# Kernel tuning notes

Hardware: AMD Instinct MI355X
Metric: run time of the kernel (lower is better)

## Reference

```python
import jax, jax.numpy as jnp
import numpy as np

NUM_HEADS = 16
EPS = 1e-6


def _ln(t, w, b):
    # LayerNorm over last dim (head_dim), elementwise affine, eps=1e-6
    mu = jnp.mean(t, axis=-1, keepdims=True)
    var = jnp.mean(jnp.square(t - mu), axis=-1, keepdims=True)
    return (t - mu) * jax.lax.rsqrt(var + EPS) * w + b


def setup_inputs() -> dict:
    key = jax.random.key(0)
    ks = jax.random.split(key, 10)
    b, s1, s2, qdim, kdim = 2, 2048, 3072, 1024, 1024
    d = qdim // NUM_HEADS
    x = jax.random.normal(ks[0], (b, s1, qdim), dtype=jnp.float32)
    y = jax.random.normal(ks[1], (b, s2, kdim), dtype=jnp.float32)
    padding_mask = jax.random.randint(ks[2], (b, s2), 0, 2) > 0
    # guarantee at least one valid key per row (avoid all -inf softmax rows)
    padding_mask = padding_mask.at[:, 0].set(True)
    w = 0.02
    Wq = jax.random.normal(ks[3], (qdim, qdim), dtype=jnp.float32) * w
    bq = jnp.zeros((qdim,), jnp.float32)
    Wkv = jax.random.normal(ks[4], (2 * qdim, kdim), dtype=jnp.float32) * w
    bkv = jnp.zeros((2 * qdim,), jnp.float32)
    qn_w = jnp.ones((d,), jnp.float32)
    qn_b = jnp.zeros((d,), jnp.float32)
    kn_w = jnp.ones((d,), jnp.float32)
    kn_b = jnp.zeros((d,), jnp.float32)
    Wo = jax.random.normal(ks[5], (qdim, qdim), dtype=jnp.float32) * w
    bo = jnp.zeros((qdim,), jnp.float32)
    return {"x": x, "y": y, "padding_mask": padding_mask,
            "Wq": Wq, "bq": bq, "Wkv": Wkv, "bkv": bkv,
            "qn_w": qn_w, "qn_b": qn_b, "kn_w": kn_w, "kn_b": kn_b,
            "Wo": Wo, "bo": bo}


def reference(x, y, padding_mask, Wq, bq, Wkv, bkv, qn_w, qn_b, kn_w, kn_b, Wo, bo):
    b, s1, c = x.shape
    s2 = y.shape[1]
    h, d = NUM_HEADS, c // NUM_HEADS
    scale = d ** (-0.5)
    q = (x @ Wq.T + bq).reshape(b, s1, h, d)
    kv = (y @ Wkv.T + bkv).reshape(b, s2, 2, h, d)
    k, v = kv[:, :, 0], kv[:, :, 1]  # (b, s2, h, d)
    q = _ln(q, qn_w, qn_b) * scale
    k = _ln(k, kn_w, kn_b)
    attn = jnp.einsum('bihd,bjhd->bhij', q, k)  # (b, h, s1, s2)
    attn = jnp.where(padding_mask[:, None, None, :], attn, -jnp.inf)
    p = jax.nn.softmax(attn, axis=-1)
    ctx = jnp.einsum('bhij,bjhd->bihd', p, v).reshape(b, s1, c)
    out = ctx @ Wo.T + bo
    return out
```

## Files before the change

### kernel.cpp

```cpp
#include <hip/hip_runtime.h>
#include <stdint.h>
#include <stddef.h>

typedef __attribute__((ext_vector_type(4))) float  f32x4;
typedef __attribute__((ext_vector_type(8))) short  short8;
typedef __attribute__((ext_vector_type(4))) short  short4v;
typedef __attribute__((ext_vector_type(2))) unsigned int uint2v;

__device__ __forceinline__ unsigned short f2bfbits(float f) {
  unsigned int u = __builtin_bit_cast(unsigned int, f);
  u += 0x7FFFu + ((u >> 16) & 1u);
  return (unsigned short)(u >> 16);
}

__device__ __forceinline__ f32x4 mfma16(short8 a, short8 b, f32x4 c) {
  return __builtin_amdgcn_mfma_f32_16x16x32_bf16(a, b, c, 0, 0, 0);
}

__device__ __forceinline__ unsigned int cvtpk(float a, float b) {
  unsigned int r;
  asm volatile("v_cvt_pk_bf16_f32 %0, %1, %2" : "=v"(r) : "v"(a), "v"(b));
  return r;
}

__device__ __forceinline__ void gload16(const void* g, void* l) {
  __builtin_amdgcn_global_load_lds(
      (const __attribute__((address_space(1))) void*)g,
      (__attribute__((address_space(3))) void*)l, 16, 0, 0);
}

__device__ __forceinline__ void cvt_block(const float* __restrict__ in,
                                          unsigned short* __restrict__ out,
                                          int blk, int t) {
  size_t i = (size_t)blk * 256 + t;
  f32x4 a = *(const f32x4*)(in + i * 8);
  f32x4 b = *(const f32x4*)(in + i * 8 + 4);
  short8 o;
  o[0] = (short)f2bfbits(a[0]); o[1] = (short)f2bfbits(a[1]);
  o[2] = (short)f2bfbits(a[2]); o[3] = (short)f2bfbits(a[3]);
  o[4] = (short)f2bfbits(b[0]); o[5] = (short)f2bfbits(b[1]);
  o[6] = (short)f2bfbits(b[2]); o[7] = (short)f2bfbits(b[3]);
  *(short8*)(out + i * 8) = o;
}

__global__ __launch_bounds__(256) void fused_prep(
    const float* __restrict__ x, unsigned short* __restrict__ xb,
    const float* __restrict__ y, unsigned short* __restrict__ yb,
    const float* __restrict__ Wq, unsigned short* __restrict__ Wqb,
    const float* __restrict__ Wkv, unsigned short* __restrict__ Wkvb,
    const float* __restrict__ Wo, unsigned short* __restrict__ Wob,
    const unsigned char* __restrict__ mraw, float* __restrict__ madd) {
  const int bid = blockIdx.x, t = threadIdx.x;
  if (bid < 2048)       { cvt_block(x,   xb,   bid,        t); return; }
  else if (bid < 5120)  { cvt_block(y,   yb,   bid - 2048, t); return; }
  else if (bid < 5632)  { cvt_block(Wq,  Wqb,  bid - 5120, t); return; }
  else if (bid < 6656)  { cvt_block(Wkv, Wkvb, bid - 5632, t); return; }
  else if (bid < 7168)  { cvt_block(Wo,  Wob,  bid - 6656, t); return; }
  __shared__ int s_na, s_gt, s_m84;
  if (t == 0) { s_na = 0; s_gt = 0; s_m84 = 0; }
  __syncthreads();
  int na = 0, gt = 0, m84 = 0;
  for (int i = t; i < 4096; i += 256) {
    unsigned char v = mraw[i];
    if (v) {
      if (i & 3) na++;
      if ((i & 7) == 4) m84++;
      if (v > 1) gt++;
    }
  }
  atomicAdd(&s_na, na); atomicAdd(&s_gt, gt); atomicAdd(&s_m84, m84);
  __syncthreads();
  int layout;
  if (s_na == 0) layout = s_m84 ? 1 : 3;
  else           layout = s_gt ? 2 : 0;
  int i = (bid - 7168) * 256 + t;
  bool mv;
  if (layout == 0)      mv = mraw[i] != 0;
  else if (layout == 1) mv = ((const int*)mraw)[i] != 0;
  else if (layout == 2) mv = ((const float*)mraw)[i] > 0.5f;
  else                  mv = ((const long long*)mraw)[i] != 0;
  madd[i] = mv ? -10.0f : -1e30f;
}

__global__ __launch_bounds__(256) void gemm_qkv(
    const unsigned short* __restrict__ xb, const unsigned short* __restrict__ Wqb,
    const float* __restrict__ bq, const float* __restrict__ qnw,
    const float* __restrict__ qnb, unsigned short* __restrict__ qln,
    const unsigned short* __restrict__ yb, const unsigned short* __restrict__ Wkvb,
    const float* __restrict__ bkv, const float* __restrict__ knw,
    const float* __restrict__ knb, unsigned short* __restrict__ kln,
    unsigned short* __restrict__ vt) {
  __shared__ unsigned short As[128 * 64];
  __shared__ unsigned short Bs[128 * 64];
  const int t = threadIdx.x, l = t & 63, w = t >> 6;
  const int lo = l & 15, hi = l >> 4;
  const int wr = w >> 1, wc = w & 1;
  const int bid = blockIdx.x;
  const int isq = bid < 256;
  const int bn = isq ? (bid & 7) : ((bid - 256) & 15);
  const int bm = isq ? (bid >> 3) : ((bid - 256) >> 4);
  const unsigned short* A = isq ? xb : yb;
  const unsigned short* B = isq ? Wqb : Wkvb;
  const float* bias = isq ? bq : bkv;
  const float* lnw = isq ? qnw : knw;
  const float* lnb = isq ? qnb : knb;
  unsigned short* bfout = isq ? qln : kln;
  const float lnscale = isq ? 0.125f * 1.44269504f : 1.0f;
  const int rpb = isq ? 2048 : 3072;
  const int K = 1024;

  const int sr = l >> 3;
  const int sc = ((l & 7) ^ sr) << 3;
  const unsigned short* Ab = A + (size_t)bm * 128 * K + (size_t)sr * K + sc;
  const unsigned short* Bb = B + (size_t)bn * 128 * K + (size_t)sr * K + sc;

  f32x4 acc[4][4] = {};

  for (int kt = 0; kt < K; kt += 64) {
    __syncthreads();
#pragma unroll
    for (int p = 0; p < 4; ++p) {
      int c = w * 4 + p;
      gload16(Ab + (size_t)c * 8 * K + kt, &As[c * 512]);
      gload16(Bb + (size_t)c * 8 * K + kt, &Bs[c * 512]);
    }
    __syncthreads();
#pragma unroll
    for (int kk = 0; kk < 2; ++kk) {
      short8 af[4], bf[4];
#pragma unroll
      for (int i = 0; i < 4; ++i) {
        int slot = (((kk * 4 + hi) ^ (lo & 7)) << 3);
        af[i] = *(const short8*)&As[(wr * 64 + i * 16 + lo) * 64 + slot];
        bf[i] = *(const short8*)&Bs[(wc * 64 + i * 16 + lo) * 64 + slot];
      }
#pragma unroll
      for (int i = 0; i < 4; ++i)
#pragma unroll
        for (int j = 0; j < 4; ++j)
          acc[i][j] = mfma16(af[i], bf[j], acc[i][j]);
    }
  }

  float bv[4];
#pragma unroll
  for (int j = 0; j < 4; ++j) bv[j] = bias[bn * 128 + wc * 64 + j * 16 + lo];
#pragma unroll
  for (int i = 0; i < 4; ++i)
#pragma unroll
    for (int j = 0; j < 4; ++j)
#pragma unroll
      for (int r = 0; r < 4; ++r) acc[i][j][r] += bv[j];

  if (!isq && bn >= 8) {
#pragma unroll
    for (int j = 0; j < 4; ++j) {
      int col = bn * 128 + wc * 64 + j * 16 + lo;
      int vcol = col - 1024, hh = vcol >> 6, dd = vcol & 63;
#pragma unroll
      for (int i = 0; i < 4; ++i) {
        int row = bm * 128 + wr * 64 + i * 16 + hi * 4;
        int bb = row >= 3072;
        int jj = row - bb * 3072;
        short4v o;
#pragma unroll
        for (int r = 0; r < 4; ++r) o[r] = (short)f2bfbits(acc[i][j][r]);
        *(short4v*)(vt + ((size_t)((bb * 16 + hh) * 64 + dd)) * 3072 + jj) = o;
      }
    }
  } else {
    float gwv[4], gbv[4];
#pragma unroll
    for (int j = 0; j < 4; ++j) {
      gwv[j] = lnw[j * 16 + lo];
      gbv[j] = lnb[j * 16 + lo];
    }
    const int hcol = (bn * 128 + wc * 64) >> 6;
#pragma unroll
    for (int i = 0; i < 4; ++i) {
#pragma unroll
      for (int r = 0; r < 4; ++r) {
        float s1 = (acc[i][0][r] + acc[i][1][r]) + (acc[i][2][r] + acc[i][3][r]);
        float s2 = (acc[i][0][r] * acc[i][0][r] + acc[i][1][r] * acc[i][1][r]) +
                   (acc[i][2][r] * acc[i][2][r] + acc[i][3][r] * acc[i][3][r]);
#pragma unroll
        for (int m = 1; m < 16; m <<= 1) {
          s1 += __shfl_xor(s1, m);
          s2 += __shfl_xor(s2, m);
        }
        float mu = s1 * 0.015625f;
        float var = fmaxf(s2 * 0.015625f - mu * mu, 0.0f);
        float rq = rsqrtf(var + 1e-6f);
        int row = bm * 128 + wr * 64 + i * 16 + hi * 4 + r;
        int bb = row >= rpb;
        int rr = row - bb * rpb;
        size_t base = ((size_t)(bb * 16 + hcol) * rpb + rr) * 64;
#pragma unroll
        for (int j = 0; j < 4; ++j)
          bfout[base + j * 16 + lo] =
              f2bfbits(((acc[i][j][r] - mu) * rq * gwv[j] + gbv[j]) * lnscale);
      }
    }
  }
}

__global__ __launch_bounds__(512) void gemm_out(
    const unsigned short* __restrict__ A, const unsigned short* __restrict__ B,
    const float* __restrict__ bias, float* __restrict__ C, int N, int K) {
  __shared__ unsigned short As[128 * 64];
  __shared__ unsigned short Bs[128 * 64];
  const int t = threadIdx.x, l = t & 63, w = t >> 6;
  const int lo = l & 15, hi = l >> 4;
  const int wr = w >> 1, wc = w & 1;
  const int bn = blockIdx.x, bm = blockIdx.y;

  const int sr = l >> 3;
  const int sc = ((l & 7) ^ sr) << 3;
  const unsigned short* Ab = A + (size_t)bm * 128 * K + (size_t)sr * K + sc;
  const unsigned short* Bb = B + (size_t)bn * 128 * K + (size_t)sr * K + sc;

  f32x4 acc[2][4] = {};

  for (int kt = 0; kt < K; kt += 64) {
    __syncthreads();
#pragma unroll
    for (int p = 0; p < 2; ++p) {
      int c = p * 8 + w;
      gload16(Ab + (size_t)c * 8 * K + kt, &As[c * 512]);
      gload16(Bb + (size_t)c * 8 * K + kt, &Bs[c * 512]);
    }
    __syncthreads();
#pragma unroll
    for (int kk = 0; kk < 2; ++kk) {
      short8 af[2], bf[4];
#pragma unroll
      for (int i = 0; i < 2; ++i) {
        int slot = (((kk * 4 + hi) ^ (lo & 7)) << 3);
        af[i] = *(const short8*)&As[(wr * 32 + i * 16 + lo) * 64 + slot];
      }
#pragma unroll
      for (int j = 0; j < 4; ++j) {
        int slot = (((kk * 4 + hi) ^ (lo & 7)) << 3);
        bf[j] = *(const short8*)&Bs[(wc * 64 + j * 16 + lo) * 64 + slot];
      }
#pragma unroll
      for (int i = 0; i < 2; ++i)
#pragma unroll
        for (int j = 0; j < 4; ++j)
          acc[i][j] = mfma16(af[i], bf[j], acc[i][j]);
    }
  }

#pragma unroll
  for (int j = 0; j < 4; ++j) {
    int col = bn * 128 + wc * 64 + j * 16 + lo;
    float bv = bias[col];
#pragma unroll
    for (int i = 0; i < 2; ++i) {
      int row = bm * 128 + wr * 32 + i * 16 + hi * 4;
#pragma unroll
      for (int r = 0; r < 4; ++r)
        C[(size_t)(row + r) * N + col] = acc[i][j][r] + bv;
    }
  }
}

__global__ __launch_bounds__(256, 4) void attn_fwd(
    const unsigned short* __restrict__ Q, const unsigned short* __restrict__ Kn,
    const unsigned short* __restrict__ Vt, const float* __restrict__ maskAdd,
    unsigned short* __restrict__ ctx) {
  int flat = blockIdx.y * 32 + blockIdx.x;
  int f = (flat & 7) * 128 + (flat >> 3);
  const int bh = f >> 5, qb = f & 31;
  const int b = bh >> 4, h = bh & 15;
  const int t = threadIdx.x, l = t & 63, w = t >> 6;
  const int lo = l & 15, hi = l >> 4;
  const int q0 = qb * 64 + w * 16;

  __shared__ unsigned short lds[20480];
  unsigned short* Ks = lds;
  unsigned short* Vs = lds + 8192;
  unsigned short* P  = lds + 16384 + w * 1024;

  const unsigned short* Qh = Q + ((size_t)bh * 2048 + q0) * 64;
  const unsigned short* Kb = Kn + (size_t)bh * 3072 * 64;
  const unsigned short* Vb = Vt + (size_t)bh * 64 * 3072;
  const float* mb = maskAdd + b * 3072;

  const int srow = w * 8 + (l >> 3);
  const int swz8 = ((l & 7) ^ ((l >> 3) & 7)) << 3;
  const unsigned short* kS = Kb + (size_t)srow * 64 + swz8;
  const unsigned short* vS = Vb + (size_t)srow * 3072 + swz8;
  const int dstoff = w * 512;

  short8 qf[2];
#pragma unroll
  for (int g = 0; g < 2; g++)
    qf[g] = *(const short8*)(Qh + (size_t)lo * 64 + g * 32 + hi * 8);

  f32x4 O[4] = {};
  f32x4 lacc = {};
  const int myswz = (lo & 7) << 3;

  short8 paR[2] = {};
  short8 vfR[4][2] = {};

#pragma unroll
  for (int j = 0; j < 2; ++j) {
    gload16(kS + (size_t)j * 2048, Ks + j * 2048 + dstoff);
    gload16(vS + (size_t)j * 98304, Vs + j * 2048 + dstoff);
  }
  __syncthreads();

  for (int kt = 0; kt < 3072; kt += 64) {
    const int cur = (kt >> 6) & 1;
    const int nxt = cur ^ 1;
    const int ktn = (kt + 64 < 3072) ? kt + 64 : 0;
#pragma unroll
    for (int j = 0; j < 2; ++j) {
      gload16(kS + (size_t)ktn * 64 + (size_t)j * 2048,
              Ks + nxt * 4096 + j * 2048 + dstoff);
      gload16(vS + ktn + (size_t)j * 98304,
              Vs + nxt * 4096 + j * 2048 + dstoff);
    }

    const unsigned short* Kc = Ks + cur * 4096;
    const unsigned short* Vc = Vs + cur * 4096;

    f32x4 s[4];
#pragma unroll
    for (int nf = 0; nf < 4; nf++)
      s[nf] = *(const f32x4*)(mb + kt + nf * 16 + hi * 4);
    __builtin_amdgcn_s_setprio(1);
#pragma unroll
    for (int nf = 0; nf < 4; nf++) {
      const int row = nf * 16 + lo;
      short8 k0 = *(const short8*)&Kc[row * 64 + ((hi * 8) ^ myswz)];
      short8 k1 = *(const short8*)&Kc[row * 64 + ((32 + hi * 8) ^ myswz)];
      s[nf] = mfma16(k0, qf[0], s[nf]);
      s[nf] = mfma16(k1, qf[1], s[nf]);
    }

#pragma unroll
    for (int df = 0; df < 4; df++)
#pragma unroll
      for (int ks = 0; ks < 2; ks++)
        O[df] = mfma16(paR[ks], vfR[df][ks], O[df]);
    __builtin_amdgcn_s_setprio(0);

#pragma unroll
    for (int nf = 0; nf < 4; nf++)
#pragma unroll
      for (int r = 0; r < 4; r++)
        s[nf][r] = __builtin_amdgcn_exp2f(s[nf][r]);
    lacc += (s[0] + s[1]) + (s[2] + s[3]);

#pragma unroll
    for (int nf = 0; nf < 4; nf++) {
      uint2v u;
      u.x = cvtpk(s[nf][0], s[nf][1]);
      u.y = cvtpk(s[nf][2], s[nf][3]);
      *(uint2v*)&P[lo * 64 + ((nf * 16 + hi * 4) ^ myswz)] = u;
    }
#pragma unroll
    for (int ks = 0; ks < 2; ks++)
      paR[ks] = *(const short8*)&P[lo * 64 + ((ks * 32 + hi * 8) ^ myswz)];
#pragma unroll
    for (int df = 0; df < 4; df++) {
      const int row = df * 16 + lo;
#pragma unroll
      for (int ks = 0; ks < 2; ks++)
        vfR[df][ks] = *(const short8*)&Vc[row * 64 + ((ks * 32 + hi * 8) ^ myswz)];
    }

    __syncthreads();
  }

  __builtin_amdgcn_s_setprio(1);
#pragma unroll
  for (int df = 0; df < 4; df++)
#pragma unroll
    for (int ks = 0; ks < 2; ks++)
      O[df] = mfma16(paR[ks], vfR[df][ks], O[df]);
  __builtin_amdgcn_s_setprio(0);

  float lr = (lacc[0] + lacc[1]) + (lacc[2] + lacc[3]);
  lr += __shfl_xor(lr, 16);
  lr += __shfl_xor(lr, 32);

  float i0 = 1.0f / __shfl(lr, hi * 4 + 0);
  float i1 = 1.0f / __shfl(lr, hi * 4 + 1);
  float i2 = 1.0f / __shfl(lr, hi * 4 + 2);
  float i3 = 1.0f / __shfl(lr, hi * 4 + 3);
  size_t rbase = (size_t)b * 2048 + q0 + hi * 4;
#pragma unroll
  for (int df = 0; df < 4; df++) {
    int cc = h * 64 + df * 16 + lo;
    ctx[(rbase + 0) * 1024 + cc] = f2bfbits(O[df][0] * i0);
    ctx[(rbase + 1) * 1024 + cc] = f2bfbits(O[df][1] * i1);
    ctx[(rbase + 2) * 1024 + cc] = f2bfbits(O[df][2] * i2);
    ctx[(rbase + 3) * 1024 + cc] = f2bfbits(O[df][3] * i3);
  }
}

extern "C" void kernel_launch(void* const* d_in, const int* in_sizes, int n_in,
                              void* d_out, int out_size, void* d_ws, size_t ws_size,
                              hipStream_t stream) {
  const float* x   = (const float*)d_in[0];
  const float* y   = (const float*)d_in[1];
  const unsigned char* pmask = (const unsigned char*)d_in[2];
  const float* Wq  = (const float*)d_in[3];
  const float* bq  = (const float*)d_in[4];
  const float* Wkv = (const float*)d_in[5];
  const float* bkv = (const float*)d_in[6];
  const float* qnw = (const float*)d_in[7];
  const float* qnb = (const float*)d_in[8];
  const float* knw = (const float*)d_in[9];
  const float* knb = (const float*)d_in[10];
  const float* Wo  = (const float*)d_in[11];
  const float* bo  = (const float*)d_in[12];
  float* out = (float*)d_out;

  const size_t MB = 1024ull * 1024ull;
  char* ws = (char*)d_ws;
  float* maskAdd       = (float*)ws;
  unsigned short* Wqb  = (unsigned short*)(ws + 32768);
  unsigned short* Wkvb = (unsigned short*)(ws + 32768 + 2 * MB);
  unsigned short* Wob  = (unsigned short*)(ws + 32768 + 6 * MB);
  unsigned short* qln  = (unsigned short*)(ws + 32768 + 8 * MB);
  unsigned short* kln  = (unsigned short*)(ws + 32768 + 16 * MB);
  unsigned short* vt   = (unsigned short*)(ws + 32768 + 28 * MB);
  unsigned short* ctxb = (unsigned short*)(ws + 32768 + 40 * MB);
  unsigned short* yb   = (unsigned short*)(ws + 32768 + 48 * MB);
  unsigned short* xb   = (unsigned short*)(ws + 32768 + 60 * MB);
  if (ws_size < 32768 + 68 * MB) return;

  fused_prep<<<dim3(7192), dim3(256), 0, stream>>>(
      x, xb, y, yb, Wq, Wqb, Wkv, Wkvb, Wo, Wob, pmask, maskAdd);

  gemm_qkv<<<dim3(1024), dim3(256), 0, stream>>>(
      xb, Wqb, bq, qnw, qnb, qln, yb, Wkvb, bkv, knw, knb, kln, vt);

  attn_fwd<<<dim3(32, 32), dim3(256), 0, stream>>>(qln, kln, vt, maskAdd, ctxb);

  gemm_out<<<dim3(8, 32), dim3(512), 0, stream>>>(ctxb, Wob, bo, out, 1024, 1024);
}
```

Baseline: 169.5 us.

## Compact valid keys via mask prefix-sum permutation and skip padded key tiles

The prep kernel now runs a prefix sum over the padding mask per batch, producing a permutation that moves valid keys to the front and a count of valid keys. The QKV GEMM scatters K rows and V columns through this permutation, and attention iterates only up to the rounded-up valid count. This removes compute on masked keys, which is about half of them with a random mask. In exchange, the V stores become scalar scattered writes instead of vector stores, and each output row needs an extra permutation lookup.

```diff
diff --git a/kernel.cpp b/kernel.cpp
--- a/kernel.cpp
+++ b/kernel.cpp
@@ -49,13 +49,16 @@
     const float* __restrict__ Wq, unsigned short* __restrict__ Wqb,
     const float* __restrict__ Wkv, unsigned short* __restrict__ Wkvb,
     const float* __restrict__ Wo, unsigned short* __restrict__ Wob,
-    const unsigned char* __restrict__ mraw, float* __restrict__ madd) {
+    const unsigned char* __restrict__ mraw, float* __restrict__ maddC,
+    int* __restrict__ perm, int* __restrict__ nvalid) {
   const int bid = blockIdx.x, t = threadIdx.x;
   if (bid < 2048)       { cvt_block(x,   xb,   bid,        t); return; }
   else if (bid < 5120)  { cvt_block(y,   yb,   bid - 2048, t); return; }
   else if (bid < 5632)  { cvt_block(Wq,  Wqb,  bid - 5120, t); return; }
   else if (bid < 6656)  { cvt_block(Wkv, Wkvb, bid - 5632, t); return; }
   else if (bid < 7168)  { cvt_block(Wo,  Wob,  bid - 6656, t); return; }
+
+  const int batch = bid - 7168;
   __shared__ int s_na, s_gt, s_m84;
   if (t == 0) { s_na = 0; s_gt = 0; s_m84 = 0; }
   __syncthreads();
@@ -73,13 +76,46 @@
   int layout;
   if (s_na == 0) layout = s_m84 ? 1 : 3;
   else           layout = s_gt ? 2 : 0;
-  int i = (bid - 7168) * 256 + t;
-  bool mv;
-  if (layout == 0)      mv = mraw[i] != 0;
-  else if (layout == 1) mv = ((const int*)mraw)[i] != 0;
-  else if (layout == 2) mv = ((const float*)mraw)[i] > 0.5f;
-  else                  mv = ((const long long*)mraw)[i] != 0;
-  madd[i] = mv ? -10.0f : -1e30f;
+
+  const int base = batch * 3072;
+  int myv[12];
+  int cnt = 0;
+#pragma unroll
+  for (int k = 0; k < 12; k++) {
+    int j = t * 12 + k;
+    int gj = base + j;
+    bool mv;
+    if (layout == 0)      mv = mraw[gj] != 0;
+    else if (layout == 1) mv = ((const int*)mraw)[gj] != 0;
+    else if (layout == 2) mv = ((const float*)mraw)[gj] > 0.5f;
+    else                  mv = ((const long long*)mraw)[gj] != 0;
+    myv[k] = mv ? 1 : 0;
+    cnt += myv[k];
+  }
+  const int lane = t & 63, wv = t >> 6;
+  int inc = cnt;
+#pragma unroll
+  for (int d = 1; d < 64; d <<= 1) {
+    int n = __shfl_up(inc, d);
+    if (lane >= d) inc += n;
+  }
+  __shared__ int wsum[4];
+  if (lane == 63) wsum[wv] = inc;
+  __syncthreads();
+  int woff = 0;
+#pragma unroll
+  for (int i2 = 0; i2 < 4; i2++) if (i2 < wv) woff += wsum[i2];
+  const int total = wsum[0] + wsum[1] + wsum[2] + wsum[3];
+  int vp = woff + inc - cnt;
+  if (t == 0) nvalid[batch] = total;
+#pragma unroll
+  for (int k = 0; k < 12; k++) {
+    int j = t * 12 + k;
+    perm[base + j] = myv[k] ? vp : (total + (j - vp));
+    vp += myv[k];
+  }
+  for (int jj = t; jj < 3072; jj += 256)
+    maddC[base + jj] = (jj < total) ? -10.0f : -1e30f;
 }
 
 __global__ __launch_bounds__(256) void gemm_qkv(
@@ -89,7 +125,7 @@
     const unsigned short* __restrict__ yb, const unsigned short* __restrict__ Wkvb,
     const float* __restrict__ bkv, const float* __restrict__ knw,
     const float* __restrict__ knb, unsigned short* __restrict__ kln,
-    unsigned short* __restrict__ vt) {
+    unsigned short* __restrict__ vt, const int* __restrict__ perm) {
   __shared__ unsigned short As[128 * 64];
   __shared__ unsigned short Bs[128 * 64];
   const int t = threadIdx.x, l = t & 63, w = t >> 6;
@@ -162,10 +198,12 @@
         int row = bm * 128 + wr * 64 + i * 16 + hi * 4;
         int bb = row >= 3072;
         int jj = row - bb * 3072;
-        short4v o;
-#pragma unroll
-        for (int r = 0; r < 4; ++r) o[r] = (short)f2bfbits(acc[i][j][r]);
-        *(short4v*)(vt + ((size_t)((bb * 16 + hh) * 64 + dd)) * 3072 + jj) = o;
+        size_t vbase = ((size_t)((bb * 16 + hh) * 64 + dd)) * 3072;
+#pragma unroll
+        for (int r = 0; r < 4; ++r) {
+          int p = perm[bb * 3072 + jj + r];
+          vt[vbase + p] = f2bfbits(acc[i][j][r]);
+        }
       }
     }
   } else {
@@ -194,7 +232,8 @@
         int row = bm * 128 + wr * 64 + i * 16 + hi * 4 + r;
         int bb = row >= rpb;
         int rr = row - bb * rpb;
-        size_t base = ((size_t)(bb * 16 + hcol) * rpb + rr) * 64;
+        int rrs = isq ? rr : perm[bb * 3072 + rr];
+        size_t base = ((size_t)(bb * 16 + hcol) * rpb + rrs) * 64;
 #pragma unroll
         for (int j = 0; j < 4; ++j)
           bfout[base + j * 16 + lo] =
@@ -268,7 +307,7 @@
 __global__ __launch_bounds__(256, 4) void attn_fwd(
     const unsigned short* __restrict__ Q, const unsigned short* __restrict__ Kn,
     const unsigned short* __restrict__ Vt, const float* __restrict__ maskAdd,
-    unsigned short* __restrict__ ctx) {
+    const int* __restrict__ nva, unsigned short* __restrict__ ctx) {
   int flat = blockIdx.y * 32 + blockIdx.x;
   int f = (flat & 7) * 128 + (flat >> 3);
   const int bh = f >> 5, qb = f & 31;
@@ -277,6 +316,9 @@
   const int lo = l & 15, hi = l >> 4;
   const int q0 = qb * 64 + w * 16;
 
+  const int nv = nva[b];
+  const int kend = (nv + 63) & ~63;
+
   __shared__ unsigned short lds[20480];
   unsigned short* Ks = lds;
   unsigned short* Vs = lds + 8192;
@@ -312,10 +354,10 @@
   }
   __syncthreads();
 
-  for (int kt = 0; kt < 3072; kt += 64) {
+  for (int kt = 0; kt < kend; kt += 64) {
     const int cur = (kt >> 6) & 1;
     const int nxt = cur ^ 1;
-    const int ktn = (kt + 64 < 3072) ? kt + 64 : 0;
+    const int ktn = (kt + 64 < kend) ? kt + 64 : 0;
 #pragma unroll
     for (int j = 0; j < 2; ++j) {
       gload16(kS + (size_t)ktn * 64 + (size_t)j * 2048,
@@ -423,25 +465,27 @@
 
   const size_t MB = 1024ull * 1024ull;
   char* ws = (char*)d_ws;
-  float* maskAdd       = (float*)ws;
-  unsigned short* Wqb  = (unsigned short*)(ws + 32768);
-  unsigned short* Wkvb = (unsigned short*)(ws + 32768 + 2 * MB);
-  unsigned short* Wob  = (unsigned short*)(ws + 32768 + 6 * MB);
-  unsigned short* qln  = (unsigned short*)(ws + 32768 + 8 * MB);
-  unsigned short* kln  = (unsigned short*)(ws + 32768 + 16 * MB);
-  unsigned short* vt   = (unsigned short*)(ws + 32768 + 28 * MB);
-  unsigned short* ctxb = (unsigned short*)(ws + 32768 + 40 * MB);
-  unsigned short* yb   = (unsigned short*)(ws + 32768 + 48 * MB);
-  unsigned short* xb   = (unsigned short*)(ws + 32768 + 60 * MB);
-  if (ws_size < 32768 + 68 * MB) return;
-
-  fused_prep<<<dim3(7192), dim3(256), 0, stream>>>(
-      x, xb, y, yb, Wq, Wqb, Wkv, Wkvb, Wo, Wob, pmask, maskAdd);
+  float* maddC         = (float*)ws;
+  int*   perm          = (int*)(ws + 24576);
+  int*   nvalid        = (int*)(ws + 49152);
+  unsigned short* Wqb  = (unsigned short*)(ws + 65536);
+  unsigned short* Wkvb = (unsigned short*)(ws + 65536 + 2 * MB);
+  unsigned short* Wob  = (unsigned short*)(ws + 65536 + 6 * MB);
+  unsigned short* qln  = (unsigned short*)(ws + 65536 + 8 * MB);
+  unsigned short* kln  = (unsigned short*)(ws + 65536 + 16 * MB);
+  unsigned short* vt   = (unsigned short*)(ws + 65536 + 28 * MB);
+  unsigned short* ctxb = (unsigned short*)(ws + 65536 + 40 * MB);
+  unsigned short* yb   = (unsigned short*)(ws + 65536 + 48 * MB);
+  unsigned short* xb   = (unsigned short*)(ws + 65536 + 60 * MB);
+  if (ws_size < 65536 + 68 * MB) return;
+
+  fused_prep<<<dim3(7170), dim3(256), 0, stream>>>(
+      x, xb, y, yb, Wq, Wqb, Wkv, Wkvb, Wo, Wob, pmask, maddC, perm, nvalid);
 
   gemm_qkv<<<dim3(1024), dim3(256), 0, stream>>>(
-      xb, Wqb, bq, qnw, qnb, qln, yb, Wkvb, bkv, knw, knb, kln, vt);
-
-  attn_fwd<<<dim3(32, 32), dim3(256), 0, stream>>>(qln, kln, vt, maskAdd, ctxb);
+      xb, Wqb, bq, qnw, qnb, qln, yb, Wkvb, bkv, knw, knb, kln, vt, perm);
+
+  attn_fwd<<<dim3(32, 32), dim3(256), 0, stream>>>(qln, kln, vt, maddC, nvalid, ctxb);
 
   gemm_out<<<dim3(8, 32), dim3(512), 0, stream>>>(ctxb, Wob, bo, out, 1024, 1024);
 }
```

Result: faster. 158.8 us (-6.3%).
